# Optimization experiments

Hardware: AMD Instinct MI355X
Metric: run time of the kernel (lower is better)

## Reference

```python
import jax, jax.numpy as jnp
import numpy as np

B, F, D, U = 4096, 32, 64, 256


def setup_inputs() -> dict:
    key = jax.random.key(0)
    k1, k2, k3, k4 = jax.random.split(key, 4)
    embeds = jax.random.normal(k1, (B, F, D), dtype=jnp.float32)
    # glorot-ish scaling for the learned weights
    linear_w = jax.random.normal(k2, (F * D, U), dtype=jnp.float32) * (2.0 / (F * D + U)) ** 0.5
    inner_w = jax.random.normal(k3, (U, F), dtype=jnp.float32) * (2.0 / (U + F)) ** 0.5
    outer_w = jax.random.normal(k4, (U, D, D), dtype=jnp.float32) * (2.0 / (2 * D)) ** 0.5
    return {"embeds": embeds, "linear_w": linear_w, "inner_w": inner_w, "outer_w": outer_w}


def reference(embeds, linear_w, inner_w, outer_w):
    b = embeds.shape[0]
    # linear signal lz: flatten fields and project -> [B, U]
    lz = embeds.reshape(b, -1) @ linear_w
    # inner products: per unit u, delta_u = sum_f w_{u,f} * e_f  -> [B, U, D];
    # lp_inner[b,u] = ||delta_u||^2 (collapses the per-unit TF loop into one einsum)
    delta = jnp.einsum('bfd,uf->bud', embeds, inner_w)
    lp_inner = jnp.sum(jnp.square(delta), axis=2)  # [B, U]
    # outer products: product = fs fs^T with fs = sum_f e_f; lp_outer[b,u] = <product_b, W_u>
    fs = jnp.sum(embeds, axis=1)  # [B, D]
    lp_outer = jnp.einsum('bi,bj,uij->bu', fs, fs, outer_w)  # [B, U]
    return jnp.concatenate([lz, lp_inner, lp_outer], axis=1)  # [B, 3U]
```

## Files before the change

### kernel.cpp

```cpp
#include <hip/hip_runtime.h>
#include <hip/hip_bf16.h>


#define KA 3072
#define KW 7168

typedef __attribute__((ext_vector_type(8))) short short8v;
typedef __attribute__((ext_vector_type(4))) float f32x4;

#define GLOAD(src, dst) __builtin_amdgcn_global_load_lds( \
    (const __attribute__((address_space(1))) void*)(src), \
    (__attribute__((address_space(3))) void*)(dst), 16, 0, 0)

static __device__ __forceinline__ short f2bf(float f) {
    union { float f; unsigned u; } v; v.f = f;
    unsigned r = v.u + 0x7fffu + ((v.u >> 16) & 1u);
    return (short)(r >> 16);
}
static __device__ __forceinline__ float bf2f(short s) {
    union { unsigned u; float f; } v; v.u = ((unsigned)(unsigned short)s) << 16;
    return v.f;
}
static __device__ __forceinline__ int cvtpk(float lo, float hi) {
    int r;
    asm("v_cvt_pk_bf16_f32 %0, %1, %2" : "=v"(r) : "v"(lo), "v"(hi));
    return r;
}

__global__ __launch_bounds__(256) void prep(const float* __restrict__ embeds,
                                            const float* __restrict__ lw,
                                            const float* __restrict__ iw,
                                            const float* __restrict__ ow,
                                            short* __restrict__ A,
                                            short* __restrict__ FS,
                                            short* __restrict__ Wt,
                                            float4* __restrict__ outv) {
    __shared__ float se[2048];
    __shared__ short sebf[2048];
    int t = threadIdx.x;

    if (blockIdx.x >= 4352) {
        size_t i = (size_t)(blockIdx.x - 4352) * 256 + t;
        #pragma unroll
        for (int r = 0; r < 3; ++r)
            outv[i + (size_t)r * 262144] = (float4){0.f, 0.f, 0.f, 0.f};
        return;
    }

    if (blockIdx.x < 4096) {
        int b = blockIdx.x;
        const float* e = embeds + (size_t)b * 2048;
        short* arow = A + (size_t)b * KA;

        float4 v0 = ((const float4*)e)[t * 2];
        float4 v1 = ((const float4*)e)[t * 2 + 1];
        ((float4*)se)[t * 2] = v0;
        ((float4*)se)[t * 2 + 1] = v1;
        short8v sb;
        sb[0] = f2bf(v0.x); sb[1] = f2bf(v0.y); sb[2] = f2bf(v0.z); sb[3] = f2bf(v0.w);
        sb[4] = f2bf(v1.x); sb[5] = f2bf(v1.y); sb[6] = f2bf(v1.z); sb[7] = f2bf(v1.w);
        ((short8v*)sebf)[t] = sb;
        *(short8v*)&arow[t * 8] = sb;

        __syncthreads();
        if (t < 64) {
            float s = 0.f;
            #pragma unroll
            for (int f = 0; f < 32; ++f) s += se[f * 64 + t];
            FS[(size_t)b * 64 + t] = f2bf(s);
        }

        int wid = t >> 6, lane = t & 63;
        int tm = wid >> 1, tn = wid & 1;
        int lr = lane & 15, lk = (lane >> 4) * 8;
        f32x4 g = {0.f, 0.f, 0.f, 0.f};
        #pragma unroll
        for (int ks = 0; ks < 2; ++ks) {
            short8v a  = *(const short8v*)&sebf[(tm * 16 + lr) * 64 + ks * 32 + lk];
            short8v bb = *(const short8v*)&sebf[(tn * 16 + lr) * 64 + ks * 32 + lk];
            g = __builtin_amdgcn_mfma_f32_16x16x32_bf16(a, bb, g, 0, 0, 0);
        }
        #pragma unroll
        for (int r = 0; r < 4; ++r) {
            int grow = tm * 16 + (lane >> 4) * 4 + r;
            int gcol = tn * 16 + lr;
            arow[2048 + grow * 32 + gcol] = f2bf(g[r]);
        }
    } else {
        int u = blockIdx.x - 4096;
        short* w = Wt + (size_t)u * KW;

        for (int k = t; k < 2048; k += 256) w[k] = f2bf(lw[(size_t)k * 256 + u]);

        if (t < 32) se[t] = iw[u * 32 + t];
        __syncthreads();
        for (int idx = t; idx < 1024; idx += 256)
            w[2048 + idx] = f2bf(se[idx >> 5] * se[idx & 31]);

        const float* owu = ow + (size_t)u * 4096;
        for (int i = t; i < 512; i += 256) {
            float4 a = ((const float4*)owu)[i * 2];
            float4 b = ((const float4*)owu)[i * 2 + 1];
            short8v s;
            s[0] = f2bf(a.x); s[1] = f2bf(a.y); s[2] = f2bf(a.z); s[3] = f2bf(a.w);
            s[4] = f2bf(b.x); s[5] = f2bf(b.y); s[6] = f2bf(b.z); s[7] = f2bf(b.w);
            *(short8v*)&w[3072 + i * 8] = s;
        }
    }
}

__global__ __launch_bounds__(256) void gemm_tile(const short* __restrict__ A,
                                                 const short* __restrict__ Wt,
                                                 const short* __restrict__ FS,
                                                 float* __restrict__ out) {
    __shared__ short As[2][8192];
    __shared__ short Bs[2][4096];

    int id = blockIdx.x;
    int xcd = id & 7, s = id >> 3;
    int mtl = s & 3, part = s >> 2;
    int ck = part >> 2, nt = part & 3;
    int mt = xcd * 4 + mtl;
    int seg, kc;
    if (ck < 2)       { seg = 0; kc = ck; }
    else if (ck == 2) { seg = 1; kc = 0; }
    else              { seg = 2; kc = ck - 3; }
    const int nk = 16;
    int brow = mt * 128, bcol = nt * 64;
    int akoff = (seg == 0) ? kc * 1024 : 2048;
    int boff  = (seg == 0) ? kc * 1024 : (seg == 1) ? 2048 : 3072 + kc * 1024;

    int t = threadIdx.x, w = t >> 6, lane = t & 63;
    int lr = lane & 15, hi = lane >> 4;
    int srow = t >> 3;
    int soct = (t & 7) ^ (srow & 7);

    const short* Asrc = A  + (size_t)(brow + srow) * KA + akoff + soct * 8;
    const short* Bsrc = Wt + (size_t)(bcol + srow) * KW + boff  + soct * 8;
    const short* Fsrc = FS + (size_t)(brow + srow) * 64 + soct * 8;

    auto stageA = [&](int p, int kt) {
        #pragma unroll
        for (int i = 0; i < 4; ++i)
            GLOAD(Asrc + (size_t)i * 32 * KA + kt * 64, &As[p][i * 2048 + t * 8]);
    };
    auto stageB = [&](int p, int kt) {
        #pragma unroll
        for (int i = 0; i < 2; ++i)
            GLOAD(Bsrc + (size_t)i * 32 * KW + kt * 64, &Bs[p][i * 2048 + t * 8]);
    };

    f32x4 acc[2][4];
    #pragma unroll
    for (int m = 0; m < 2; ++m)
        #pragma unroll
        for (int n = 0; n < 4; ++n) acc[m][n] = (f32x4){0.f, 0.f, 0.f, 0.f};

    auto compute = [&](const short* a_s, const short* b_s) {
        #pragma unroll
        for (int ks = 0; ks < 2; ++ks) {
            int oct = ((ks * 4 + hi) ^ (lr & 7)) * 8;
            short8v a[2], b[4];
            #pragma unroll
            for (int m = 0; m < 2; ++m)
                a[m] = *(const short8v*)&a_s[(w * 32 + m * 16 + lr) * 64 + oct];
            #pragma unroll
            for (int n = 0; n < 4; ++n)
                b[n] = *(const short8v*)&b_s[(n * 16 + lr) * 64 + oct];
            __builtin_amdgcn_s_setprio(1);
            #pragma unroll
            for (int m = 0; m < 2; ++m)
                #pragma unroll
                for (int n = 0; n < 4; ++n)
                    acc[m][n] = __builtin_amdgcn_mfma_f32_16x16x32_bf16(a[m], b[n], acc[m][n], 0, 0, 0);
            __builtin_amdgcn_s_setprio(0);
        }
    };

    if (seg != 2) {
        stageA(0, 0); stageB(0, 0);
        stageA(1, 1); stageB(1, 1);
        __builtin_amdgcn_sched_barrier(0);
        for (int kt = 0; kt < nk; ++kt) {
            int cur = kt & 1;
            if (kt + 1 < nk) asm volatile("s_waitcnt vmcnt(6)" ::: "memory");
            else             asm volatile("s_waitcnt vmcnt(0)" ::: "memory");
            __builtin_amdgcn_s_barrier();
            __builtin_amdgcn_sched_barrier(0);
            compute(As[cur], Bs[cur]);
            __builtin_amdgcn_sched_barrier(0);
            __builtin_amdgcn_s_barrier();
            if (kt + 2 < nk) { stageA(cur, kt + 2); stageB(cur, kt + 2); }
            __builtin_amdgcn_sched_barrier(0);
        }
    } else {
        #pragma unroll
        for (int i = 0; i < 4; ++i)
            GLOAD(Fsrc + (size_t)i * 32 * 64, &As[0][i * 2048 + t * 8]);
        stageB(0, 0); stageB(1, 1);
        asm volatile("s_waitcnt vmcnt(4)" ::: "memory");
        __builtin_amdgcn_s_barrier();
        __builtin_amdgcn_sched_barrier(0);

        float fj[2][2][8];
        #pragma unroll
        for (int m = 0; m < 2; ++m)
            #pragma unroll
            for (int ks = 0; ks < 2; ++ks) {
                int oct = ((ks * 4 + hi) ^ (lr & 7)) * 8;
                short8v v = *(const short8v*)&As[0][(w * 32 + m * 16 + lr) * 64 + oct];
                #pragma unroll
                for (int e = 0; e < 8; ++e) fj[m][ks][e] = bf2f(v[e]);
            }
        for (int kt = 0; kt < nk; ++kt) {
            int cur = kt & 1;
            if (kt + 1 < nk) asm volatile("s_waitcnt vmcnt(2)" ::: "memory");
            else             asm volatile("s_waitcnt vmcnt(0)" ::: "memory");
            __builtin_amdgcn_s_barrier();
            __builtin_amdgcn_sched_barrier(0);
            int iidx = kc * 16 + kt;
            int ioff = ((iidx >> 3) ^ (lr & 7)) * 8 + (iidx & 7);
            float sv[2];
            #pragma unroll
            for (int m = 0; m < 2; ++m)
                sv[m] = bf2f(As[0][(w * 32 + m * 16 + lr) * 64 + ioff]);
            #pragma unroll
            for (int ks = 0; ks < 2; ++ks) {
                int oct = ((ks * 4 + hi) ^ (lr & 7)) * 8;
                short8v b[4];
                #pragma unroll
                for (int n = 0; n < 4; ++n)
                    b[n] = *(const short8v*)&Bs[cur][(n * 16 + lr) * 64 + oct];
                #pragma unroll
                for (int m = 0; m < 2; ++m) {
                    union { int i32[4]; short8v v; } fa;
                    #pragma unroll
                    for (int q2 = 0; q2 < 4; ++q2)
                        fa.i32[q2] = cvtpk(sv[m] * fj[m][ks][2 * q2], sv[m] * fj[m][ks][2 * q2 + 1]);
                    __builtin_amdgcn_s_setprio(1);
                    #pragma unroll
                    for (int n = 0; n < 4; ++n)
                        acc[m][n] = __builtin_amdgcn_mfma_f32_16x16x32_bf16(fa.v, b[n], acc[m][n], 0, 0, 0);
                    __builtin_amdgcn_s_setprio(0);
                }
            }
            __builtin_amdgcn_sched_barrier(0);
            __builtin_amdgcn_s_barrier();
            if (kt + 2 < nk) stageB(cur, kt + 2);
            __builtin_amdgcn_sched_barrier(0);
        }
    }

    int segbase = seg * 256;
    #pragma unroll
    for (int m = 0; m < 2; ++m) {
        int row0 = brow + w * 32 + m * 16 + hi * 4;
        #pragma unroll
        for (int n = 0; n < 4; ++n) {
            int col = segbase + bcol + n * 16 + lr;
            #pragma unroll
            for (int r = 0; r < 4; ++r)
                unsafeAtomicAdd(&out[(size_t)(row0 + r) * 768 + col], acc[m][n][r]);
        }
    }
}

extern "C" void kernel_launch(void* const* d_in, const int* in_sizes, int n_in,
                              void* d_out, int out_size, void* d_ws, size_t ws_size,
                              hipStream_t stream) {
    const float* embeds = (const float*)d_in[0];
    const float* lw = (const float*)d_in[1];
    const float* iw = (const float*)d_in[2];
    const float* ow = (const float*)d_in[3];
    float* out = (float*)d_out;

    short* A  = (short*)d_ws;
    short* Wt = A + (size_t)4096 * KA;
    short* FS = Wt + (size_t)256 * KW;

    prep<<<dim3(5376), dim3(256), 0, stream>>>(embeds, lw, iw, ow, A, FS, Wt, (float4*)out);
    gemm_tile<<<dim3(896), dim3(256), 0, stream>>>(A, Wt, FS, out);
}
```

Measured before the change: 62.67 us.

## Enlarge GEMM tiles to 128x128 and store fs transposed per tile

```diff
diff --git a/kernel.cpp b/kernel.cpp
--- a/kernel.cpp
+++ b/kernel.cpp
@@ -32,7 +32,7 @@
                                             const float* __restrict__ iw,
                                             const float* __restrict__ ow,
                                             short* __restrict__ A,
-                                            short* __restrict__ FS,
+                                            short* __restrict__ FST,
                                             short* __restrict__ Wt,
                                             float4* __restrict__ outv) {
     __shared__ float se[2048];
@@ -67,7 +67,7 @@
             float s = 0.f;
             #pragma unroll
             for (int f = 0; f < 32; ++f) s += se[f * 64 + t];
-            FS[(size_t)b * 64 + t] = f2bf(s);
+            FST[((size_t)(b >> 7)) * 8192 + t * 128 + (b & 127)] = f2bf(s);
         }
 
         int wid = t >> 6, lane = t & 63;
@@ -109,35 +109,35 @@
     }
 }
 
-__global__ __launch_bounds__(256) void gemm_tile(const short* __restrict__ A,
-                                                 const short* __restrict__ Wt,
-                                                 const short* __restrict__ FS,
-                                                 float* __restrict__ out) {
+__global__ __launch_bounds__(256, 2) void gemm_tile(const short* __restrict__ A,
+                                                    const short* __restrict__ Wt,
+                                                    const short* __restrict__ FST,
+                                                    float* __restrict__ out) {
     __shared__ short As[2][8192];
-    __shared__ short Bs[2][4096];
+    __shared__ short Bs[2][8192];
 
     int id = blockIdx.x;
     int xcd = id & 7, s = id >> 3;
-    int mtl = s & 3, part = s >> 2;
-    int ck = part >> 2, nt = part & 3;
-    int mt = xcd * 4 + mtl;
-    int seg, kc;
-    if (ck < 2)       { seg = 0; kc = ck; }
-    else if (ck == 2) { seg = 1; kc = 0; }
-    else              { seg = 2; kc = ck - 3; }
-    const int nk = 16;
-    int brow = mt * 128, bcol = nt * 64;
-    int akoff = (seg == 0) ? kc * 1024 : 2048;
-    int boff  = (seg == 0) ? kc * 1024 : (seg == 1) ? 2048 : 3072 + kc * 1024;
+    int mt = xcd * 4 + (s & 3);
+    int sc = s >> 2;
+    int c = sc & 7, nt = sc >> 3;
+    int seg, kc, nk;
+    if (c < 2)      { seg = 0; kc = c;     nk = 16; }
+    else if (c < 4) { seg = 1; kc = c - 2; nk = 8;  }
+    else            { seg = 2; kc = c - 4; nk = 16; }
+    int brow = mt * 128, bcol = nt * 128;
+    int akoff = (seg == 0) ? kc * 1024 : 2048 + kc * 512;
+    int boff  = (seg == 0) ? kc * 1024 : (seg == 1) ? 2048 + kc * 512 : 3072 + kc * 1024;
 
     int t = threadIdx.x, w = t >> 6, lane = t & 63;
+    int wm = w >> 1, wn = w & 1;
     int lr = lane & 15, hi = lane >> 4;
     int srow = t >> 3;
     int soct = (t & 7) ^ (srow & 7);
 
     const short* Asrc = A  + (size_t)(brow + srow) * KA + akoff + soct * 8;
     const short* Bsrc = Wt + (size_t)(bcol + srow) * KW + boff  + soct * 8;
-    const short* Fsrc = FS + (size_t)(brow + srow) * 64 + soct * 8;
+    const short* Fsrc = FST + (size_t)mt * 8192;
 
     auto stageA = [&](int p, int kt) {
         #pragma unroll
@@ -146,13 +146,13 @@
     };
     auto stageB = [&](int p, int kt) {
         #pragma unroll
-        for (int i = 0; i < 2; ++i)
+        for (int i = 0; i < 4; ++i)
             GLOAD(Bsrc + (size_t)i * 32 * KW + kt * 64, &Bs[p][i * 2048 + t * 8]);
     };
 
-    f32x4 acc[2][4];
+    f32x4 acc[4][4];
     #pragma unroll
-    for (int m = 0; m < 2; ++m)
+    for (int m = 0; m < 4; ++m)
         #pragma unroll
         for (int n = 0; n < 4; ++n) acc[m][n] = (f32x4){0.f, 0.f, 0.f, 0.f};
 
@@ -160,16 +160,16 @@
         #pragma unroll
         for (int ks = 0; ks < 2; ++ks) {
             int oct = ((ks * 4 + hi) ^ (lr & 7)) * 8;
-            short8v a[2], b[4];
-            #pragma unroll
-            for (int m = 0; m < 2; ++m)
-                a[m] = *(const short8v*)&a_s[(w * 32 + m * 16 + lr) * 64 + oct];
+            short8v a[4], b[4];
+            #pragma unroll
+            for (int m = 0; m < 4; ++m)
+                a[m] = *(const short8v*)&a_s[(wm * 64 + m * 16 + lr) * 64 + oct];
             #pragma unroll
             for (int n = 0; n < 4; ++n)
-                b[n] = *(const short8v*)&b_s[(n * 16 + lr) * 64 + oct];
+                b[n] = *(const short8v*)&b_s[(wn * 64 + n * 16 + lr) * 64 + oct];
             __builtin_amdgcn_s_setprio(1);
             #pragma unroll
-            for (int m = 0; m < 2; ++m)
+            for (int m = 0; m < 4; ++m)
                 #pragma unroll
                 for (int n = 0; n < 4; ++n)
                     acc[m][n] = __builtin_amdgcn_mfma_f32_16x16x32_bf16(a[m], b[n], acc[m][n], 0, 0, 0);
@@ -183,7 +183,7 @@
         __builtin_amdgcn_sched_barrier(0);
         for (int kt = 0; kt < nk; ++kt) {
             int cur = kt & 1;
-            if (kt + 1 < nk) asm volatile("s_waitcnt vmcnt(6)" ::: "memory");
+            if (kt + 1 < nk) asm volatile("s_waitcnt vmcnt(8)" ::: "memory");
             else             asm volatile("s_waitcnt vmcnt(0)" ::: "memory");
             __builtin_amdgcn_s_barrier();
             __builtin_amdgcn_sched_barrier(0);
@@ -196,43 +196,44 @@
     } else {
         #pragma unroll
         for (int i = 0; i < 4; ++i)
-            GLOAD(Fsrc + (size_t)i * 32 * 64, &As[0][i * 2048 + t * 8]);
+            GLOAD(Fsrc + i * 2048 + t * 8, &As[0][i * 2048 + t * 8]);
         stageB(0, 0); stageB(1, 1);
-        asm volatile("s_waitcnt vmcnt(4)" ::: "memory");
+        asm volatile("s_waitcnt vmcnt(8)" ::: "memory");
         __builtin_amdgcn_s_barrier();
         __builtin_amdgcn_sched_barrier(0);
 
-        float fj[2][2][8];
-        #pragma unroll
-        for (int m = 0; m < 2; ++m)
+        float fj[4][2][8];
+        #pragma unroll
+        for (int m = 0; m < 4; ++m) {
+            int row = wm * 64 + m * 16 + lr;
             #pragma unroll
             for (int ks = 0; ks < 2; ++ks) {
-                int oct = ((ks * 4 + hi) ^ (lr & 7)) * 8;
-                short8v v = *(const short8v*)&As[0][(w * 32 + m * 16 + lr) * 64 + oct];
-                #pragma unroll
-                for (int e = 0; e < 8; ++e) fj[m][ks][e] = bf2f(v[e]);
+                int j0 = (ks * 4 + hi) * 8;
+                #pragma unroll
+                for (int e = 0; e < 8; ++e)
+                    fj[m][ks][e] = bf2f(As[0][(j0 + e) * 128 + row]);
             }
+        }
         for (int kt = 0; kt < nk; ++kt) {
             int cur = kt & 1;
-            if (kt + 1 < nk) asm volatile("s_waitcnt vmcnt(2)" ::: "memory");
+            if (kt + 1 < nk) asm volatile("s_waitcnt vmcnt(4)" ::: "memory");
             else             asm volatile("s_waitcnt vmcnt(0)" ::: "memory");
             __builtin_amdgcn_s_barrier();
             __builtin_amdgcn_sched_barrier(0);
             int iidx = kc * 16 + kt;
-            int ioff = ((iidx >> 3) ^ (lr & 7)) * 8 + (iidx & 7);
-            float sv[2];
-            #pragma unroll
-            for (int m = 0; m < 2; ++m)
-                sv[m] = bf2f(As[0][(w * 32 + m * 16 + lr) * 64 + ioff]);
+            float sv[4];
+            #pragma unroll
+            for (int m = 0; m < 4; ++m)
+                sv[m] = bf2f(As[0][iidx * 128 + wm * 64 + m * 16 + lr]);
             #pragma unroll
             for (int ks = 0; ks < 2; ++ks) {
                 int oct = ((ks * 4 + hi) ^ (lr & 7)) * 8;
                 short8v b[4];
                 #pragma unroll
                 for (int n = 0; n < 4; ++n)
-                    b[n] = *(const short8v*)&Bs[cur][(n * 16 + lr) * 64 + oct];
-                #pragma unroll
-                for (int m = 0; m < 2; ++m) {
+                    b[n] = *(const short8v*)&Bs[cur][(wn * 64 + n * 16 + lr) * 64 + oct];
+                #pragma unroll
+                for (int m = 0; m < 4; ++m) {
                     union { int i32[4]; short8v v; } fa;
                     #pragma unroll
                     for (int q2 = 0; q2 < 4; ++q2)
@@ -253,11 +254,11 @@
 
     int segbase = seg * 256;
     #pragma unroll
-    for (int m = 0; m < 2; ++m) {
-        int row0 = brow + w * 32 + m * 16 + hi * 4;
+    for (int m = 0; m < 4; ++m) {
+        int row0 = brow + wm * 64 + m * 16 + hi * 4;
         #pragma unroll
         for (int n = 0; n < 4; ++n) {
-            int col = segbase + bcol + n * 16 + lr;
+            int col = segbase + bcol + wn * 64 + n * 16 + lr;
             #pragma unroll
             for (int r = 0; r < 4; ++r)
                 unsafeAtomicAdd(&out[(size_t)(row0 + r) * 768 + col], acc[m][n][r]);
@@ -274,10 +275,10 @@
     const float* ow = (const float*)d_in[3];
     float* out = (float*)d_out;
 
-    short* A  = (short*)d_ws;
-    short* Wt = A + (size_t)4096 * KA;
-    short* FS = Wt + (size_t)256 * KW;
-
-    prep<<<dim3(5376), dim3(256), 0, stream>>>(embeds, lw, iw, ow, A, FS, Wt, (float4*)out);
-    gemm_tile<<<dim3(896), dim3(256), 0, stream>>>(A, Wt, FS, out);
-}
+    short* A   = (short*)d_ws;
+    short* Wt  = A + (size_t)4096 * KA;
+    short* FST = Wt + (size_t)256 * KW;
+
+    prep<<<dim3(5376), dim3(256), 0, stream>>>(embeds, lw, iw, ow, A, FST, Wt, (float4*)out);
+    gemm_tile<<<dim3(512), dim3(256), 0, stream>>>(A, Wt, FST, out);
+}
```

Result: faster. 58.06 us (-7.4%).

## Drop split-K for linear segment and use plain stores for non-reduced outputs

Applied to the files above, without the earlier changes.

```diff
diff --git a/kernel.cpp b/kernel.cpp
--- a/kernel.cpp
+++ b/kernel.cpp
@@ -32,7 +32,7 @@
                                             const float* __restrict__ iw,
                                             const float* __restrict__ ow,
                                             short* __restrict__ A,
-                                            short* __restrict__ FS,
+                                            short* __restrict__ FST,
                                             short* __restrict__ Wt,
                                             float4* __restrict__ outv) {
     __shared__ float se[2048];
@@ -40,10 +40,9 @@
     int t = threadIdx.x;
 
     if (blockIdx.x >= 4352) {
-        size_t i = (size_t)(blockIdx.x - 4352) * 256 + t;
-        #pragma unroll
-        for (int r = 0; r < 3; ++r)
-            outv[i + (size_t)r * 262144] = (float4){0.f, 0.f, 0.f, 0.f};
+        int idx = (blockIdx.x - 4352) * 256 + t;
+        int row = idx >> 6, c4 = idx & 63;
+        outv[(size_t)row * 192 + 128 + c4] = (float4){0.f, 0.f, 0.f, 0.f};
         return;
     }
 
@@ -67,7 +66,7 @@
             float s = 0.f;
             #pragma unroll
             for (int f = 0; f < 32; ++f) s += se[f * 64 + t];
-            FS[(size_t)b * 64 + t] = f2bf(s);
+            FST[((size_t)(b >> 7)) * 8192 + t * 128 + (b & 127)] = f2bf(s);
         }
 
         int wid = t >> 6, lane = t & 63;
@@ -111,24 +110,21 @@
 
 __global__ __launch_bounds__(256) void gemm_tile(const short* __restrict__ A,
                                                  const short* __restrict__ Wt,
-                                                 const short* __restrict__ FS,
+                                                 const short* __restrict__ FST,
                                                  float* __restrict__ out) {
     __shared__ short As[2][8192];
     __shared__ short Bs[2][4096];
 
     int id = blockIdx.x;
     int xcd = id & 7, s = id >> 3;
-    int mtl = s & 3, part = s >> 2;
-    int ck = part >> 2, nt = part & 3;
+    int seg, mtl, nt, kc, nk;
+    if (s < 16)      { seg = 0; mtl = s & 3;  nt = s >> 2;        kc = 0;       nk = 32; }
+    else if (s < 32) { int q = s - 16; seg = 1; mtl = q & 3; nt = q >> 2;       kc = 0;  nk = 16; }
+    else             { int q = s - 32; seg = 2; mtl = q & 3; nt = (q >> 2) & 3; kc = q >> 4; nk = 16; }
     int mt = xcd * 4 + mtl;
-    int seg, kc;
-    if (ck < 2)       { seg = 0; kc = ck; }
-    else if (ck == 2) { seg = 1; kc = 0; }
-    else              { seg = 2; kc = ck - 3; }
-    const int nk = 16;
     int brow = mt * 128, bcol = nt * 64;
-    int akoff = (seg == 0) ? kc * 1024 : 2048;
-    int boff  = (seg == 0) ? kc * 1024 : (seg == 1) ? 2048 : 3072 + kc * 1024;
+    int akoff = (seg == 0) ? 0 : 2048;
+    int boff  = (seg == 0) ? 0 : (seg == 1) ? 2048 : 3072 + kc * 1024;
 
     int t = threadIdx.x, w = t >> 6, lane = t & 63;
     int lr = lane & 15, hi = lane >> 4;
@@ -137,7 +133,7 @@
 
     const short* Asrc = A  + (size_t)(brow + srow) * KA + akoff + soct * 8;
     const short* Bsrc = Wt + (size_t)(bcol + srow) * KW + boff  + soct * 8;
-    const short* Fsrc = FS + (size_t)(brow + srow) * 64 + soct * 8;
+    const short* Fsrc = FST + (size_t)mt * 8192;
 
     auto stageA = [&](int p, int kt) {
         #pragma unroll
@@ -196,7 +192,7 @@
     } else {
         #pragma unroll
         for (int i = 0; i < 4; ++i)
-            GLOAD(Fsrc + (size_t)i * 32 * 64, &As[0][i * 2048 + t * 8]);
+            GLOAD(Fsrc + i * 2048 + t * 8, &As[0][i * 2048 + t * 8]);
         stageB(0, 0); stageB(1, 1);
         asm volatile("s_waitcnt vmcnt(4)" ::: "memory");
         __builtin_amdgcn_s_barrier();
@@ -204,14 +200,16 @@
 
         float fj[2][2][8];
         #pragma unroll
-        for (int m = 0; m < 2; ++m)
+        for (int m = 0; m < 2; ++m) {
+            int row = w * 32 + m * 16 + lr;
             #pragma unroll
             for (int ks = 0; ks < 2; ++ks) {
-                int oct = ((ks * 4 + hi) ^ (lr & 7)) * 8;
-                short8v v = *(const short8v*)&As[0][(w * 32 + m * 16 + lr) * 64 + oct];
-                #pragma unroll
-                for (int e = 0; e < 8; ++e) fj[m][ks][e] = bf2f(v[e]);
-            }
+                int j0 = (ks * 4 + hi) * 8;
+                #pragma unroll
+                for (int e = 0; e < 8; ++e)
+                    fj[m][ks][e] = bf2f(As[0][(j0 + e) * 128 + row]);
+            }
+        }
         for (int kt = 0; kt < nk; ++kt) {
             int cur = kt & 1;
             if (kt + 1 < nk) asm volatile("s_waitcnt vmcnt(2)" ::: "memory");
@@ -219,11 +217,10 @@
             __builtin_amdgcn_s_barrier();
             __builtin_amdgcn_sched_barrier(0);
             int iidx = kc * 16 + kt;
-            int ioff = ((iidx >> 3) ^ (lr & 7)) * 8 + (iidx & 7);
             float sv[2];
             #pragma unroll
             for (int m = 0; m < 2; ++m)
-                sv[m] = bf2f(As[0][(w * 32 + m * 16 + lr) * 64 + ioff]);
+                sv[m] = bf2f(As[0][iidx * 128 + w * 32 + m * 16 + lr]);
             #pragma unroll
             for (int ks = 0; ks < 2; ++ks) {
                 int oct = ((ks * 4 + hi) ^ (lr & 7)) * 8;
@@ -252,15 +249,29 @@
     }
 
     int segbase = seg * 256;
-    #pragma unroll
-    for (int m = 0; m < 2; ++m) {
-        int row0 = brow + w * 32 + m * 16 + hi * 4;
-        #pragma unroll
-        for (int n = 0; n < 4; ++n) {
-            int col = segbase + bcol + n * 16 + lr;
-            #pragma unroll
-            for (int r = 0; r < 4; ++r)
-                unsafeAtomicAdd(&out[(size_t)(row0 + r) * 768 + col], acc[m][n][r]);
+    if (seg != 2) {
+        #pragma unroll
+        for (int m = 0; m < 2; ++m) {
+            int row0 = brow + w * 32 + m * 16 + hi * 4;
+            #pragma unroll
+            for (int n = 0; n < 4; ++n) {
+                int col = segbase + bcol + n * 16 + lr;
+                #pragma unroll
+                for (int r = 0; r < 4; ++r)
+                    out[(size_t)(row0 + r) * 768 + col] = acc[m][n][r];
+            }
+        }
+    } else {
+        #pragma unroll
+        for (int m = 0; m < 2; ++m) {
+            int row0 = brow + w * 32 + m * 16 + hi * 4;
+            #pragma unroll
+            for (int n = 0; n < 4; ++n) {
+                int col = segbase + bcol + n * 16 + lr;
+                #pragma unroll
+                for (int r = 0; r < 4; ++r)
+                    unsafeAtomicAdd(&out[(size_t)(row0 + r) * 768 + col], acc[m][n][r]);
+            }
         }
     }
 }
@@ -274,10 +285,10 @@
     const float* ow = (const float*)d_in[3];
     float* out = (float*)d_out;
 
-    short* A  = (short*)d_ws;
-    short* Wt = A + (size_t)4096 * KA;
-    short* FS = Wt + (size_t)256 * KW;
-
-    prep<<<dim3(5376), dim3(256), 0, stream>>>(embeds, lw, iw, ow, A, FS, Wt, (float4*)out);
-    gemm_tile<<<dim3(896), dim3(256), 0, stream>>>(A, Wt, FS, out);
-}
+    short* A   = (short*)d_ws;
+    short* Wt  = A + (size_t)4096 * KA;
+    short* FST = Wt + (size_t)256 * KW;
+
+    prep<<<dim3(5376), dim3(256), 0, stream>>>(embeds, lw, iw, ow, A, FST, Wt, (float4*)out);
+    gemm_tile<<<dim3(768), dim3(256), 0, stream>>>(A, Wt, FST, out);
+}
```

Result: faster. 56.33 us (-10.1%).
